# Kernel optimization log

Hardware: AMD Instinct MI355X
Metric: run time of the kernel (lower is better)

The kernel has to match this reference:

```python
import jax, jax.numpy as jnp
import numpy as np

ALPHA = 0.1       # args.alpha
T = 1.0           # args.T temperature
SIGMA = 64.0      # Gaussian kernel bandwidth of kernel_function
B_CONST = 1.0     # B in get_lambda
N_ITERS = 50      # 2^-50 << tol=1e-8, matches the break condition of the 1000-iter loop
HW = 256          # image resolution (upsample target)


def _features(feat):
    # get_feature: bilinear upsample (align_corners=False == half-pixel, as jax.image.resize) then sigmoid(x/T)
    n, c, _, _ = feat.shape
    up = jax.image.resize(feat, (n, c, HW, HW), method='bilinear')
    return jax.nn.sigmoid(up / T)


def setup_inputs() -> dict:
    key = jax.random.key(0)
    k1, k2, k3, k4 = jax.random.split(key, 4)
    return {
        'cal_feat': jax.random.normal(k1, (256, 1, 64, 64), jnp.float32),
        'test_feat': jax.random.normal(k2, (32, 1, 64, 64), jnp.float32),
        'cal_gt': jax.random.randint(k3, (256, 1, 256, 256), 0, 2, jnp.int32),
        'test_gt': jax.random.randint(k4, (32, 1, 256, 256), 0, 2, jnp.int32),
    }


def reference(cal_feat, test_feat, cal_gt, test_gt):
    cal_res = _features(cal_feat)    # [N,1,H,W] in (0,1)
    test_res = _features(test_feat)  # [B,1,H,W]
    N = cal_res.shape[0]
    B = test_res.shape[0]
    f32 = cal_res.dtype

    # kernel_function.get_weight: Gaussian RBF on flattened features, plus self-weight 1, row-normalized -> [B, N+1]
    cf = cal_res.reshape(N, -1)
    tf = test_res.reshape(B, -1)
    d2 = (tf * tf).sum(-1)[:, None] + (cf * cf).sum(-1)[None, :] - 2.0 * (tf @ cf.T)
    k = jnp.exp(-d2 / (2.0 * SIGMA * SIGMA))
    w = jnp.concatenate([k, jnp.ones((B, 1), f32)], axis=1)
    w = w / w.sum(axis=1, keepdims=True)

    # FNR_i(t) = #{positive pixels of cal sample i with score < t} / #positives
    # (pred = res >= t, so false negatives are positive pixels with res < t). Precompute sorted
    # positive-pixel scores per cal sample so the bisection is a batched searchsorted.
    gt = (cal_gt > 0).reshape(N, -1)
    pos = jnp.sum(gt, axis=1)                                    # [N]
    scores = jnp.where(gt, cal_res.reshape(N, -1), jnp.inf)
    sorted_scores = jnp.sort(scores, axis=1)                     # [N, HW*HW], padding at +inf
    pos_f = jnp.maximum(pos, 1).astype(f32)

    def fnr_at(t):  # t: [B] thresholds -> [N, B]
        cnt = jax.vmap(lambda s: jnp.searchsorted(s, t, side='left'))(sorted_scores)
        return cnt.astype(f32) / pos_f[:, None]

    # batched bisection on lambda (get_lambda, vectorized over the B test samples)
    def body(carry, _):
        low, high = carry
        lam = 0.5 * (low + high)
        fnr = fnr_at(1.0 - lam)                                   # [N, B]
        risk = jnp.einsum('bn,nb->b', w[:, :-1], fnr) + w[:, -1] * B_CONST
        high = jnp.where(risk < ALPHA, lam, high)
        low = jnp.where(risk >= ALPHA, lam, low)
        return (low, high), None

    init = (jnp.zeros((B,), f32), jnp.ones((B,), f32))
    (low, _), _ = jax.lax.scan(body, init, None, length=N_ITERS)
    lam = low  # _lambda = low after the loop

    # prediction set, size and per-test FNR (get_fnr_list on the test sample)
    pred = test_res >= (1.0 - lam)[:, None, None, None]           # [B,1,H,W] bool
    size = jnp.sum(pred, axis=(1, 2, 3)).astype(f32)
    tgt = test_gt > 0
    tp = jnp.sum(pred & tgt, axis=(1, 2, 3)).astype(f32)
    tpos = jnp.maximum(jnp.sum(tgt, axis=(1, 2, 3)), 1).astype(f32)
    fnr_test = 1.0 - tp / tpos                                    # fdr_tensor, [B]
    return fnr_test, lam, size
```

## Files before the change

### kernel.cpp

```cpp
#include <hip/hip_runtime.h>


#define NPIX 65536
#define HB 16256
#define CDF_STRIDE 16272
#define ALPHA 0.1f
#define STAGE_CAP 35840

#define OFF_TESTRES  0
#define OFF_CALBF    8388608u
#define OFF_TESTBF   41943040u
#define OFF_GROUPED  46137344u
#define OFF_CDF      79691776u
#define OFF_GPART    88023040u
#define OFF_CC       90120192u
#define OFF_THR      90121216u
#define OFF_LAM      90121344u
#define OFF_FACC     90121472u

typedef __attribute__((ext_vector_type(8))) short bf16x8;
typedef __attribute__((ext_vector_type(16))) float f32x16;

__device__ __forceinline__ unsigned short f2bf_rne(float f) {
  unsigned u = __float_as_uint(f);
  return (unsigned short)((u + 0x7FFFu + ((u >> 16) & 1u)) >> 16);
}

__device__ __forceinline__ int SW(int w) { return w ^ ((w >> 5) & 31); }

__device__ __forceinline__ float sig_v(float a, float b, float wy) {
  float v = a * (1.f - wy) + b * wy;
  return 1.f / (1.f + __expf(-v));
}

__global__ __launch_bounds__(1024, 2) void k_calt(const float* __restrict__ featc,
                                                  const int* __restrict__ gt,
                                                  unsigned short* __restrict__ calbf,
                                                  unsigned short* __restrict__ cdf,
                                                  unsigned short* __restrict__ grouped,
                                                  float* __restrict__ cc,
                                                  const float* __restrict__ featt,
                                                  float* __restrict__ tres,
                                                  unsigned short* __restrict__ tbf) {
  __shared__ unsigned smem[17313];
  __shared__ float sfeat[4096];
  __shared__ __align__(16) unsigned short sstage[STAGE_CAP];
  float* tfeat = (float*)sstage;
  const int tid = threadIdx.x;
  const int lane = tid & 63, wv = tid >> 6;
  const int x = tid & 255, yq = tid >> 8;
  float sx = 0.25f * (float)x - 0.375f;
  int x0 = (int)floorf(sx);
  float wx = sx - (float)x0;
  int x1 = x0 + 1;
  if (x0 < 0) x0 = 0;
  if (x1 > 63) x1 = 63;

  const int n = blockIdx.x;
  const int b = n >> 3, sl = n & 7;
  for (int i = tid; i < HB; i += 1024) smem[i] = 0;
  for (int i = tid; i < 4096; i += 1024) {
    sfeat[i] = featc[n * 4096 + i];
    tfeat[i] = featt[b * 4096 + i];
  }
  const int* gtn = gt + (size_t)n * NPIX;
  unsigned short* cbn = calbf + (size_t)n * NPIX;
  __syncthreads();

  {
    const float* tf0 = tfeat + x0;
    const float* tf1 = tfeat + x1;
    float* resb = tres + (size_t)b * NPIX;
    unsigned short* tbn = tbf + (size_t)b * NPIX;
    const int mt0 = sl * 8 + yq * 2;
    int rp = mt0 - 1 < 0 ? 0 : mt0 - 1;
    float hp = tf0[rp * 64] * (1.f - wx) + tf1[rp * 64] * wx;
    float hc = tf0[mt0 * 64] * (1.f - wx) + tf1[mt0 * 64] * wx;
    #pragma unroll
    for (int q = 0; q < 2; ++q) {
      int m = mt0 + q;
      int rn = m + 1 > 63 ? 63 : m + 1;
      float hn = tf0[rn * 64] * (1.f - wx) + tf1[rn * 64] * wx;
      #pragma unroll
      for (int j = 0; j < 4; ++j) {
        int y = 4 * m + j;
        float sy = 0.25f * (float)y - 0.375f;
        int y0 = (int)floorf(sy);
        float wy = sy - (float)y0;
        float s = sig_v(j < 2 ? hp : hc, j < 2 ? hc : hn, wy);
        int p = (y << 8) + x;
        resb[p] = s;
        tbn[p] = f2bf_rne(s);
      }
      hp = hc; hc = hn;
    }
  }

  const float* f0 = sfeat + x0;
  const float* f1 = sfeat + x1;
  const int m0 = yq * 16;
  unsigned long long pm = 0ull;
  float sumsq = 0.f;
  {
    int rp = m0 - 1 < 0 ? 0 : m0 - 1;
    float hp = f0[rp * 64] * (1.f - wx) + f1[rp * 64] * wx;
    float hc = f0[m0 * 64] * (1.f - wx) + f1[m0 * 64] * wx;
    #pragma unroll 4
    for (int q = 0; q < 16; ++q) {
      int m = m0 + q;
      int rn = m + 1 > 63 ? 63 : m + 1;
      float hn = f0[rn * 64] * (1.f - wx) + f1[rn * 64] * wx;
      #pragma unroll
      for (int j = 0; j < 4; ++j) {
        int y = 4 * m + j;
        float sy = 0.25f * (float)y - 0.375f;
        int y0 = (int)floorf(sy);
        float wy = sy - (float)y0;
        float s = sig_v(j < 2 ? hp : hc, j < 2 ? hc : hn, wy);
        int p = (y << 8) + x;
        unsigned short bh = f2bf_rne(s);
        cbn[p] = bh;
        float sr = __uint_as_float((unsigned)bh << 16);
        sumsq += sr * sr;
        if (gtn[p] > 0) {
          pm |= (1ull << (q * 4 + j));
          atomicAdd(&smem[SW((int)(__float_as_uint(s) >> 16))], 1u);
        }
      }
      hp = hc; hc = hn;
    }
  }
  #pragma unroll
  for (int off = 32; off; off >>= 1) sumsq += __shfl_xor(sumsq, off);
  if (lane == 0) smem[16272 + wv] = __float_as_uint(sumsq);
  __syncthreads();
  if (tid == 0) {
    float c = 0.f;
    for (int w = 0; w < 16; ++w) c += __uint_as_float(smem[16272 + w]);
    cc[n] = c;
  }
  const int base = tid * 16;
  unsigned psum = 0;
  if (tid < 1016) {
    #pragma unroll
    for (int j = 0; j < 16; ++j) psum += smem[SW(base + j)];
  }
  unsigned inc = psum;
  #pragma unroll
  for (int off = 1; off < 64; off <<= 1) {
    unsigned v = __shfl_up(inc, off);
    if (lane >= off) inc += v;
  }
  if (lane == 63) smem[16256 + wv] = inc;
  smem[16288 + tid] = inc - psum;
  __syncthreads();
  {
    unsigned woff = 0;
    for (int w = 0; w < wv; ++w) woff += smem[16256 + w];
    unsigned run = woff + smem[16288 + tid];
    if (tid < 1016) {
      #pragma unroll
      for (int j = 0; j < 16; ++j) {
        int si = SW(base + j);
        unsigned h = smem[si];
        smem[si] = run;
        run += h;
      }
    }
    if (tid == 1015) smem[17312] = run;
  }
  __syncthreads();
  unsigned short* cdfn = cdf + (size_t)n * CDF_STRIDE;
  for (int i = tid; i < HB; i += 1024) cdfn[i] = (unsigned short)smem[SW(i)];
  const unsigned pos = smem[17312];
  if (tid == 0) cdfn[HB] = (unsigned short)pos;
  __syncthreads();
  unsigned short* gn = grouped + (size_t)n * NPIX;
  {
    int rp = m0 - 1 < 0 ? 0 : m0 - 1;
    float hp = f0[rp * 64] * (1.f - wx) + f1[rp * 64] * wx;
    float hc = f0[m0 * 64] * (1.f - wx) + f1[m0 * 64] * wx;
    for (int q = 0; q < 16; ++q) {
      int m = m0 + q;
      int rn = m + 1 > 63 ? 63 : m + 1;
      float hn = f0[rn * 64] * (1.f - wx) + f1[rn * 64] * wx;
      unsigned nib = (unsigned)(pm >> (q * 4)) & 0xFu;
      if (nib) {
        #pragma unroll
        for (int j = 0; j < 4; ++j) {
          if (nib & (1u << j)) {
            int y = 4 * m + j;
            float sy = 0.25f * (float)y - 0.375f;
            int y0 = (int)floorf(sy);
            float wy = sy - (float)y0;
            float s = sig_v(j < 2 ? hp : hc, j < 2 ? hc : hn, wy);
            unsigned bits = __float_as_uint(s);
            unsigned idx = atomicAdd(&smem[SW((int)(bits >> 16))], 1u);
            unsigned short lo = (unsigned short)(bits & 0xFFFFu);
            if (idx < STAGE_CAP) sstage[idx] = lo;
            else gn[idx] = lo;
          }
        }
      }
      hp = hc; hc = hn;
    }
  }
  __syncthreads();
  unsigned lim = pos < STAGE_CAP ? pos : STAGE_CAP;
  for (unsigned i = tid; i < lim; i += 1024) gn[i] = sstage[i];
}

__global__ __launch_bounds__(256) void k_gemm(const unsigned short* __restrict__ tbf,
                                              const unsigned short* __restrict__ cbf,
                                              float* __restrict__ gpart) {
  __shared__ __align__(16) unsigned short As[16384];
  __shared__ __align__(16) unsigned short Bs[16384];
  __shared__ float lred[4][1024];
  const int tid = threadIdx.x;
  const int lane = tid & 63, wv = tid >> 6;
  const int r = lane & 31, half = lane >> 5;
  const int nt = blockIdx.x;
  f32x16 acc;
  #pragma unroll
  for (int i = 0; i < 16; ++i) acc[i] = 0.f;
  for (int ch = 0; ch < 2; ++ch) {
    const size_t kbase = (size_t)blockIdx.y * 1024 + ch * 512;
    __syncthreads();
    #pragma unroll
    for (int s = 0; s < 16; ++s) {
      int flat = s * 256 + tid;
      int rem = flat & 2047;
      int row = rem >> 6, kb = rem & 63;
      const unsigned short* src = (flat >= 2048)
          ? cbf + (size_t)(nt * 32 + row) * NPIX + kbase + kb * 8
          : tbf + (size_t)row * NPIX + kbase + kb * 8;
      int slot = ((kb << 5) + row) ^ (kb & 31);
      int4 v = *(const int4*)src;
      *(int4*)((flat >= 2048 ? Bs : As) + slot * 8) = v;
    }
    __syncthreads();
    #pragma unroll
    for (int i = 0; i < 8; ++i) {
      int k8 = (wv << 4) + i * 2 + half;
      int slot = ((k8 << 5) + r) ^ (k8 & 31);
      bf16x8 a = *(const bf16x8*)(As + slot * 8);
      bf16x8 b = *(const bf16x8*)(Bs + slot * 8);
      acc = __builtin_amdgcn_mfma_f32_32x32x16_bf16(a, b, acc, 0, 0, 0);
    }
  }
  #pragma unroll
  for (int rg = 0; rg < 16; ++rg) {
    int m = (rg & 3) + 8 * (rg >> 2) + 4 * half;
    lred[wv][m * 32 + r] = acc[rg];
  }
  __syncthreads();
  float* gp = gpart + (size_t)(blockIdx.y * 8 + nt) * 1024;
  for (int e = tid; e < 1024; e += 256)
    gp[e] = lred[0][e] + lred[1][e] + lred[2][e] + lred[3][e];
}

__global__ __launch_bounds__(512) void k_quantw(const float* __restrict__ gpart,
                                                const float* __restrict__ cc,
                                                const unsigned short* __restrict__ tbf,
                                                const unsigned short* __restrict__ cdf,
                                                const unsigned short* __restrict__ grouped,
                                                float* __restrict__ lam,
                                                float* __restrict__ thr,
                                                int* __restrict__ facc) {
  __shared__ float qs[256];
  __shared__ float bins[4096];
  __shared__ float red[8];
  __shared__ float tpart[16];
  __shared__ float bc[3];
  __shared__ unsigned sBin;
  const int b = blockIdx.x, tid = threadIdx.x;
  const int lane = tid & 63, wv = tid >> 6;

  if (tid < 4) facc[b * 4 + tid] = 0;
  for (int i = tid; i < 4096; i += 512) bins[i] = 0.f;
  if (tid == 0) sBin = 0xFFFFFFFFu;

  {
    const unsigned short* tbn = tbf + (size_t)b * NPIX;
    const int xa = tid & 255, ya = tid >> 8;
    const int yb = ya + 2;
    float sa = 0.f, sb = 0.f;
    #pragma unroll 4
    for (int it = 0; it < 64; ++it) {
      float ra = __uint_as_float((unsigned)tbn[((it * 4 + ya) << 8) + xa] << 16);
      float rb = __uint_as_float((unsigned)tbn[((it * 4 + yb) << 8) + xa] << 16);
      sa += ra * ra;
      sb += rb * rb;
    }
    #pragma unroll
    for (int off = 32; off; off >>= 1) {
      sa += __shfl_xor(sa, off);
      sb += __shfl_xor(sb, off);
    }
    if (lane == 0) { tpart[wv] = sa; tpart[8 + wv] = sb; }
  }
  __syncthreads();
  if (tid == 0) {
    float t = 0.f;
    for (int w = 0; w < 16; ++w) t += tpart[w];
    bc[2] = t;
  }
  float g = 0.f;
  if (tid < 256) {
    const float* gp = gpart + ((tid >> 5) * 1024) + (b * 32) + (tid & 31);
    #pragma unroll 8
    for (int ks = 0; ks < 64; ++ks) g += gp[(size_t)ks * 8192];
  }
  __syncthreads();
  float k = 0.f;
  if (tid < 256) {
    float d2 = bc[2] + cc[tid] - 2.f * g;
    k = expf(-d2 * (1.f / 8192.f));
  }
  float v = k;
  #pragma unroll
  for (int off = 32; off; off >>= 1) v += __shfl_xor(v, off);
  if (lane == 0) red[wv] = v;
  __syncthreads();
  if (tid == 0) {
    float ws = 1.f;
    for (int w = 0; w < 8; ++w) ws += red[w];
    bc[0] = ws;
  }
  __syncthreads();
  const float wsum = bc[0];
  const float wlast = 1.f / wsum;
  const float R = ALPHA - wlast;
  if (R <= 0.f) {
    if (tid == 0) { lam[b] = 1.0f; thr[b] = 0.0f; }
    return;
  }
  if (tid < 256) {
    unsigned pos = cdf[(size_t)tid * CDF_STRIDE + HB];
    qs[tid] = k / (wsum * (float)(pos ? pos : 1u));
  }
  __syncthreads();

  int lo = 0, hi = HB;
  float baseS = 0.f;
  for (int it = 0; it < 14; ++it) {
    int mid = (lo + hi) >> 1;
    float p = 0.f;
    if (tid < 256) p = qs[tid] * (float)cdf[(size_t)tid * CDF_STRIDE + mid];
    float r = p;
    #pragma unroll
    for (int off = 32; off; off >>= 1) r += __shfl_xor(r, off);
    if (lane == 0) red[wv] = r;
    __syncthreads();
    if (tid == 0) {
      float s = 0.f;
      for (int w = 0; w < 8; ++w) s += red[w];
      bc[1] = s;
    }
    __syncthreads();
    float S = bc[1];
    if (S < R) { lo = mid; baseS = S; } else { hi = mid; }
  }
  const int B = lo;

  {
    const int n = tid >> 1;
    const float q = qs[n];
    const unsigned short* cn = cdf + (size_t)n * CDF_STRIDE;
    const unsigned short* gn = grouped + (size_t)n * NPIX;
    unsigned e0 = cn[B + 1];
    for (unsigned j = (unsigned)cn[B] + (tid & 1); j < e0; j += 2)
      atomicAdd(&bins[gn[j] >> 4], q);
  }
  __syncthreads();

  if (wv == 0) {
    float s = 0.f;
    for (int j = 0; j < 64; ++j) s += bins[lane * 64 + j];
    float inc = s;
    #pragma unroll
    for (int off = 1; off < 64; off <<= 1) {
      float u = __shfl_up(inc, off);
      if (lane >= off) inc += u;
    }
    float pre = inc - s;
    bool hit = (baseS + pre < R) && (baseS + inc >= R);
    unsigned long long m = __ballot(hit);
    int ow = m ? (__ffsll((unsigned long long)m) - 1) : -1;
    if (lane == ow) {
      float run = baseS + pre;
      unsigned bin = (unsigned)lane * 64 + 63;
      for (int j = 0; j < 64; ++j) {
        float bv = bins[lane * 64 + j];
        if (run + bv >= R) { bin = (unsigned)lane * 64 + j; break; }
        run += bv;
      }
      sBin = bin;
    }
    if (m == 0 && lane == 0) sBin = 4095u;
  }
  __syncthreads();
  if (tid == 0) {
    unsigned tb = ((unsigned)B << 16) | (sBin << 4);
    lam[b] = 1.0f - __uint_as_float(tb | 0x8u);
    thr[b] = __uint_as_float((tb | 0xFu) + 1u);
  }
}

__global__ __launch_bounds__(256) void k_finalp(const float* __restrict__ tres,
                                                const int* __restrict__ tgt,
                                                const float* __restrict__ thr,
                                                const float* __restrict__ lam,
                                                int* __restrict__ facc,
                                                float* __restrict__ out) {
  __shared__ int red[12];
  const int b = blockIdx.x, seg = blockIdx.y, tid = threadIdx.x;
  const int lane = tid & 63, wv = tid >> 6;
  const float th = thr[b];
  const float4* rb4 = (const float4*)(tres + (size_t)b * NPIX + seg * 8192);
  const int4* gb4 = (const int4*)(tgt + (size_t)b * NPIX + seg * 8192);
  int sz = 0, tp = 0, tpos = 0;
  #pragma unroll
  for (int i = 0; i < 8; ++i) {
    float4 r4 = rb4[i * 256 + tid];
    int4 g4 = gb4[i * 256 + tid];
    int p0 = (r4.x >= th), t0 = (g4.x > 0);
    int p1 = (r4.y >= th), t1 = (g4.y > 0);
    int p2 = (r4.z >= th), t2 = (g4.z > 0);
    int p3 = (r4.w >= th), t3 = (g4.w > 0);
    sz += p0 + p1 + p2 + p3;
    tp += (p0 & t0) + (p1 & t1) + (p2 & t2) + (p3 & t3);
    tpos += t0 + t1 + t2 + t3;
  }
  #pragma unroll
  for (int off = 32; off; off >>= 1) {
    sz += __shfl_xor(sz, off);
    tp += __shfl_xor(tp, off);
    tpos += __shfl_xor(tpos, off);
  }
  if (lane == 0) { red[wv] = sz; red[4 + wv] = tp; red[8 + wv] = tpos; }
  __syncthreads();
  if (tid == 0) {
    int s0 = red[0] + red[1] + red[2] + red[3];
    int s1 = red[4] + red[5] + red[6] + red[7];
    int s2 = red[8] + red[9] + red[10] + red[11];
    atomicAdd(&facc[b * 4 + 0], s0);
    atomicAdd(&facc[b * 4 + 1], s1);
    atomicAdd(&facc[b * 4 + 2], s2);
    __threadfence();
    int done = atomicAdd(&facc[b * 4 + 3], 1);
    if (done == 7) {
      int f0 = atomicAdd(&facc[b * 4 + 0], 0);
      int f1 = atomicAdd(&facc[b * 4 + 1], 0);
      int f2 = atomicAdd(&facc[b * 4 + 2], 0);
      float tposf = (float)(f2 > 0 ? f2 : 1);
      out[b] = 1.f - (float)f1 / tposf;
      out[32 + b] = lam[b];
      out[64 + b] = (float)f0;
    }
  }
}

extern "C" void kernel_launch(void* const* d_in, const int* in_sizes, int n_in,
                              void* d_out, int out_size, void* d_ws, size_t ws_size,
                              hipStream_t stream) {
  const float* cal_feat = (const float*)d_in[0];
  const float* test_feat = (const float*)d_in[1];
  const int* cal_gt = (const int*)d_in[2];
  const int* test_gt = (const int*)d_in[3];
  float* out = (float*)d_out;
  char* ws = (char*)d_ws;

  float* test_res = (float*)(ws + OFF_TESTRES);
  unsigned short* cal_bf = (unsigned short*)(ws + OFF_CALBF);
  unsigned short* test_bf = (unsigned short*)(ws + OFF_TESTBF);
  unsigned short* grouped = (unsigned short*)(ws + OFF_GROUPED);
  unsigned short* cdf = (unsigned short*)(ws + OFF_CDF);
  float* gpart = (float*)(ws + OFF_GPART);
  float* cc = (float*)(ws + OFF_CC);
  float* thr = (float*)(ws + OFF_THR);
  float* lam = (float*)(ws + OFF_LAM);
  int* facc = (int*)(ws + OFF_FACC);

  k_calt<<<dim3(256), dim3(1024), 0, stream>>>(cal_feat, cal_gt, cal_bf, cdf, grouped, cc,
                                               test_feat, test_res, test_bf);
  k_gemm<<<dim3(8, 64), dim3(256), 0, stream>>>(test_bf, cal_bf, gpart);
  k_quantw<<<dim3(32), dim3(512), 0, stream>>>(gpart, cc, test_bf, cdf, grouped,
                                               lam, thr, facc);
  k_finalp<<<dim3(32, 8), dim3(256), 0, stream>>>(test_res, test_gt, thr, lam, facc, out);
}
```

Measured before the change: 239.7 us.

## Pack ground-truth into shared bitmask and transpose CDF for coalesced bisection

Result: faster. 223.9 us (-6.6%).

```diff
diff --git a/kernel.cpp b/kernel.cpp
--- a/kernel.cpp
+++ b/kernel.cpp
@@ -17,6 +17,7 @@
 #define OFF_THR      90121216u
 #define OFF_LAM      90121344u
 #define OFF_FACC     90121472u
+#define OFF_CDFT     90122240u
 
 typedef __attribute__((ext_vector_type(8))) short bf16x8;
 typedef __attribute__((ext_vector_type(16))) float f32x16;
@@ -46,6 +47,7 @@
   __shared__ float sfeat[4096];
   __shared__ __align__(16) unsigned short sstage[STAGE_CAP];
   float* tfeat = (float*)sstage;
+  unsigned* gmask = (unsigned*)(sstage + 8192);
   const int tid = threadIdx.x;
   const int lane = tid & 63, wv = tid >> 6;
   const int x = tid & 255, yq = tid >> 8;
@@ -63,7 +65,21 @@
     sfeat[i] = featc[n * 4096 + i];
     tfeat[i] = featt[b * 4096 + i];
   }
-  const int* gtn = gt + (size_t)n * NPIX;
+  {
+    const int4* gt4 = (const int4*)(gt + (size_t)n * NPIX);
+    for (int w = tid; w < 2048; w += 1024) {
+      unsigned m = 0;
+      #pragma unroll
+      for (int j = 0; j < 8; ++j) {
+        int4 g = gt4[w * 8 + j];
+        m |= (g.x > 0 ? 1u : 0u) << (j * 4);
+        m |= (g.y > 0 ? 2u : 0u) << (j * 4);
+        m |= (g.z > 0 ? 4u : 0u) << (j * 4);
+        m |= (g.w > 0 ? 8u : 0u) << (j * 4);
+      }
+      gmask[w] = m;
+    }
+  }
   unsigned short* cbn = calbf + (size_t)n * NPIX;
   __syncthreads();
 
@@ -122,7 +138,7 @@
         cbn[p] = bh;
         float sr = __uint_as_float((unsigned)bh << 16);
         sumsq += sr * sr;
-        if (gtn[p] > 0) {
+        if ((gmask[p >> 5] >> (x & 31)) & 1u) {
           pm |= (1ull << (q * 4 + j));
           atomicAdd(&smem[SW((int)(__float_as_uint(s) >> 16))], 1u);
         }
@@ -210,6 +226,20 @@
   for (unsigned i = tid; i < lim; i += 1024) gn[i] = sstage[i];
 }
 
+__global__ __launch_bounds__(256) void k_tr(const unsigned short* __restrict__ cdf,
+                                            unsigned short* __restrict__ cdfT) {
+  __shared__ unsigned short tile[256][136];
+  const int b0 = blockIdx.x * 128;
+  const int tid = threadIdx.x;
+  const unsigned short* src = cdf + (size_t)tid * CDF_STRIDE + b0;
+  #pragma unroll
+  for (int j = 0; j < 128; j += 8)
+    *(int4*)&tile[tid][j] = *(const int4*)(src + j);
+  __syncthreads();
+  for (int j = 0; j < 128; ++j)
+    cdfT[(size_t)(b0 + j) * 256 + tid] = tile[tid][j];
+}
+
 __global__ __launch_bounds__(256) void k_gemm(const unsigned short* __restrict__ tbf,
                                               const unsigned short* __restrict__ cbf,
                                               float* __restrict__ gpart) {
@@ -263,6 +293,7 @@
                                                 const float* __restrict__ cc,
                                                 const unsigned short* __restrict__ tbf,
                                                 const unsigned short* __restrict__ cdf,
+                                                const unsigned short* __restrict__ cdfT,
                                                 const unsigned short* __restrict__ grouped,
                                                 float* __restrict__ lam,
                                                 float* __restrict__ thr,
@@ -346,7 +377,7 @@
   for (int it = 0; it < 14; ++it) {
     int mid = (lo + hi) >> 1;
     float p = 0.f;
-    if (tid < 256) p = qs[tid] * (float)cdf[(size_t)tid * CDF_STRIDE + mid];
+    if (tid < 256) p = qs[tid] * (float)cdfT[(size_t)mid * 256 + tid];
     float r = p;
     #pragma unroll
     for (int off = 32; off; off >>= 1) r += __shfl_xor(r, off);
@@ -476,6 +507,7 @@
   unsigned short* test_bf = (unsigned short*)(ws + OFF_TESTBF);
   unsigned short* grouped = (unsigned short*)(ws + OFF_GROUPED);
   unsigned short* cdf = (unsigned short*)(ws + OFF_CDF);
+  unsigned short* cdfT = (unsigned short*)(ws + OFF_CDFT);
   float* gpart = (float*)(ws + OFF_GPART);
   float* cc = (float*)(ws + OFF_CC);
   float* thr = (float*)(ws + OFF_THR);
@@ -484,8 +516,9 @@
 
   k_calt<<<dim3(256), dim3(1024), 0, stream>>>(cal_feat, cal_gt, cal_bf, cdf, grouped, cc,
                                                test_feat, test_res, test_bf);
+  k_tr<<<dim3(127), dim3(256), 0, stream>>>(cdf, cdfT);
   k_gemm<<<dim3(8, 64), dim3(256), 0, stream>>>(test_bf, cal_bf, gpart);
-  k_quantw<<<dim3(32), dim3(512), 0, stream>>>(gpart, cc, test_bf, cdf, grouped,
+  k_quantw<<<dim3(32), dim3(512), 0, stream>>>(gpart, cc, test_bf, cdf, cdfT, grouped,
                                                lam, thr, facc);
   k_finalp<<<dim3(32, 8), dim3(256), 0, stream>>>(test_res, test_gt, thr, lam, facc, out);
 }
```
